# Performance work log

Measured on AMD Instinct MI355X. Metric: run time of the kernel, lower is better.

The kernel has to match this reference:

```python
import jax, jax.numpy as jnp
import numpy as np

T, B, UNITS, ACTIONS = 128, 16, 128, 6
NORM_SCALE = float(np.sqrt(UNITS))  # norm_scale = sqrt(urnn_units)


def _conv(x, w, b, stride):
    y = jax.lax.conv_general_dilated(x, w, (stride, stride), 'VALID',
                                     dimension_numbers=('NCHW', 'OIHW', 'NCHW'))
    return jax.nn.relu(y + b[None, :, None, None])


def setup_inputs() -> dict:
    key = jax.random.key(0)
    ks = jax.random.split(key, 16)
    rn = lambda k, s, sc=0.05: jax.random.normal(k, s, jnp.float32) * sc
    return {
        'x': jax.random.uniform(ks[0], (T * B, 84, 84, 3), jnp.float32, 0.0, 255.0),
        'done': (jax.random.uniform(ks[1], (T * B,)) < 0.1).astype(jnp.float32),
        'urnn_state_real': jnp.ones((B, UNITS), jnp.float32),
        'urnn_state_imag': jnp.zeros((B, UNITS), jnp.float32),
        'conv1_w': rn(ks[2], (32, 3, 8, 8)), 'conv1_b': jnp.zeros((32,), jnp.float32),
        'conv2_w': rn(ks[3], (64, 32, 4, 4)), 'conv2_b': jnp.zeros((64,), jnp.float32),
        'conv3_w': rn(ks[4], (64, 64, 3, 3)), 'conv3_b': jnp.zeros((64,), jnp.float32),
        'fc_w': rn(ks[5], (3136, 512)), 'fc_b': jnp.zeros((512,), jnp.float32),
        'win_r': rn(ks[6], (512, UNITS)), 'win_i': rn(ks[7], (512, UNITS)),
        'wrec_r': rn(ks[8], (UNITS, UNITS)), 'wrec_i': rn(ks[9], (UNITS, UNITS)),
        'actor_w': rn(ks[10], (2 * UNITS, ACTIONS), 0.01), 'actor_b': jnp.zeros((ACTIONS,), jnp.float32),
        'critic_w': rn(ks[11], (2 * UNITS, 1)), 'critic_b': jnp.zeros((1,), jnp.float32),
    }


def reference(x, done, urnn_state_real, urnn_state_imag,
              conv1_w, conv1_b, conv2_w, conv2_b, conv3_w, conv3_b,
              fc_w, fc_b, win_r, win_i, wrec_r, wrec_i,
              actor_w, actor_b, critic_w, critic_b):
    # CNN backbone (Nature-DQN) on NHWC frames scaled to [0,1]
    h = jnp.transpose(x, (0, 3, 1, 2)) / 255.0
    h = _conv(h, conv1_w, conv1_b, 4)      # [N,32,20,20]
    h = _conv(h, conv2_w, conv2_b, 2)      # [N,64,9,9]
    h = _conv(h, conv3_w, conv3_b, 1)      # [N,64,7,7]
    h = h.reshape(h.shape[0], -1)          # [N,3136]
    h = jax.nn.relu(h @ fc_w + fc_b)       # [N,512]

    h = h.reshape(T, B, -1)
    d = done.reshape(T, B)
    win = win_r + 1j * win_i               # [512,U] complex input projection
    wrec = wrec_r + 1j * wrec_i            # [U,U] complex recurrent matrix
    init = jnp.ones((B, UNITS), jnp.complex64)  # initial_hidden, ||.|| = sqrt(U)
    state0 = (urnn_state_real + 1j * urnn_state_imag).astype(jnp.complex64)

    def step(state, hd):
        ht, dt = hd
        reset = (1.0 - dt)[:, None]
        st = reset * state + (1.0 - reset) * init   # reset-mask blending
        pre = st @ wrec + ht.astype(jnp.complex64) @ win
        norm = jnp.sqrt(jnp.sum(pre.real ** 2 + pre.imag ** 2, axis=-1, keepdims=True))
        new = pre * (NORM_SCALE / norm).astype(jnp.complex64)  # renorm to sqrt(U)
        return new, new

    _, hs = jax.lax.scan(step, state0, (h, d))      # hs: [T,B,U] complex
    hs = hs.reshape(T * B, UNITS)
    hreal = jnp.concatenate([hs.real, hs.imag], axis=-1)  # [T*B, 2U]
    logits = hreal @ actor_w + actor_b
    value = hreal @ critic_w + critic_b
    return jnp.concatenate([logits, value], axis=-1)  # [T*B, ACTIONS+1]
```

## Files before the change

kernel.cpp:

```cpp
#include <hip/hip_runtime.h>
#include <hip/hip_bf16.h>

#define N_FRAMES 2048
#define T_STEPS  128
#define BATCH    16
#define UNITS    128
#define NORM_SCALE 11.313708498984760390f

typedef short bf16x8 __attribute__((ext_vector_type(8)));
typedef float f32x4 __attribute__((ext_vector_type(4)));

static __device__ inline unsigned short f2bf(float f) {
    __hip_bfloat16 h = __float2bfloat16(f);
    return __builtin_bit_cast(unsigned short, h);
}

static const size_t OFF_W1P   = 0;
static const size_t OFF_W2P   = 6144;
static const size_t OFF_W3P   = 38912;
static const size_t OFF_FCWP  = 75776;
static const size_t OFF_WSC   = 894976;
static const size_t OFF_HSR   = 1681408;
static const size_t OFF_PROJR = 2205696;
static const size_t OFF_H     = 2729984;
static const size_t OFF_Y2    = 3778560;
static const size_t OFF_Y1    = 14395392;
static const size_t OFF_Y3    = OFF_Y1;

__global__ void permute_w1mf(const float* __restrict__ w, unsigned short* __restrict__ o) {
    int i = blockIdx.x * 256 + threadIdx.x;
    if (i >= 8192) return;
    int j = i & 7; int lane = (i >> 3) & 63; int nt = (i >> 9) & 1; int ky = i >> 10;
    int t = (lane >> 4) * 8 + j;
    int oc = nt * 16 + (lane & 15);
    float v = 0.f;
    if (t < 24) {
        int kx = t / 3, ic = t % 3;
        v = w[((oc * 3 + ic) * 8 + ky) * 8 + kx] * (1.0f / 255.0f);
    }
    o[i] = f2bf(v);
}
__global__ void permute_w2mf(const float* __restrict__ w, unsigned short* __restrict__ o) {
    int i = blockIdx.x * 256 + threadIdx.x;
    if (i >= 32768) return;
    int j = i & 7; int lane = (i >> 3) & 63; int nt = (i >> 9) & 3; int kk = i >> 11;
    int ic = (lane >> 4) * 8 + j;
    int oc = nt * 16 + (lane & 15);
    int ky = kk >> 2, kx = kk & 3;
    o[i] = f2bf(w[((oc * 32 + ic) * 4 + ky) * 4 + kx]);
}
__global__ void permute_w3mf(const float* __restrict__ w, unsigned short* __restrict__ o) {
    int i = blockIdx.x * 256 + threadIdx.x;
    if (i >= 36864) return;
    int j = i & 7; int lane = (i >> 3) & 63; int nt = (i >> 9) & 3; int c = (i >> 11) & 1; int kk = i >> 12;
    int ic = c * 32 + (lane >> 4) * 8 + j;
    int oc = nt * 16 + (lane & 15);
    int ky = kk / 3, kx = kk % 3;
    o[i] = f2bf(w[((oc * 64 + ic) * 3 + ky) * 3 + kx]);
}
__global__ void permute_fcwmf(const float* __restrict__ w, unsigned short* __restrict__ o) {
    int i = blockIdx.x * 256 + threadIdx.x;
    if (i >= 1638400) return;
    int jj = i & 7; int lane = (i >> 3) & 63; int ntg = (i >> 9) & 31; int kk = i >> 14;
    int k = kk * 32 + (lane >> 4) * 8 + jj;
    int n = ntg * 16 + (lane & 15);
    float v = 0.f;
    if (k < 3136) {
        int p = k >> 6, c = k & 63;
        v = w[(size_t)(c * 49 + p) * 512 + n];
    }
    o[i] = f2bf(v);
}
__global__ void permute_wscan(const float* __restrict__ wr, const float* __restrict__ wi,
                              unsigned short* __restrict__ o) {
    int i = blockIdx.x * 256 + threadIdx.x;
    if (i >= 32768) return;
    int j = i & 7; int lane = (i >> 3) & 63; int ks = (i >> 9) & 3; int nt = (i >> 11) & 7;
    int comp = i >> 14;
    int k = ks * 32 + (lane >> 4) * 8 + j;
    int n = nt * 16 + (lane & 15);
    const float* src = comp ? wi : wr;
    o[i] = f2bf(src[k * 128 + n]);
}

__global__ __launch_bounds__(256) void conv1_kernel(const float* __restrict__ x,
                                                    const unsigned short* __restrict__ wmf,
                                                    const float* __restrict__ b,
                                                    unsigned short* __restrict__ y) {
    __shared__ unsigned short xs[11096];
    int tid = threadIdx.x;
    int blk = blockIdx.x;
    int n = blk >> 1, hb = blk & 1;

    const float4* xb4 = reinterpret_cast<const float4*>(x + (size_t)n * 21168 + hb * 40 * 252);
#pragma unroll
    for (int it = 0; it < 11; ++it) {
        int i = it * 256 + tid;
        if (i < 2772) {
            float4 v = xb4[i];
            ushort4 h;
            h.x = f2bf(v.x); h.y = f2bf(v.y); h.z = f2bf(v.z); h.w = f2bf(v.w);
            *reinterpret_cast<ushort4*>(&xs[i * 4]) = h;
        }
    }
    if (tid < 8) xs[11088 + tid] = 0;
    __syncthreads();

    int lane = tid & 63;
    int wv = tid >> 6;
    int row = lane & 15;
    int seg = lane >> 4;
    const uint4* wm = reinterpret_cast<const uint4*>(wmf);
    float b0 = b[row];
    float b1 = b[16 + row];
    int pbase = n * 400 + hb * 200;

    for (int tile = wv; tile < 13; tile += 4) {
        int p = tile * 16 + row; if (p > 199) p = 199;
        int eb = (p / 20) * 1008 + (p % 20) * 12 + seg * 8;
        f32x4 acc0 = {0.f, 0.f, 0.f, 0.f};
        f32x4 acc1 = {0.f, 0.f, 0.f, 0.f};
#pragma unroll
        for (int ky = 0; ky < 8; ++ky) {
            int ea = eb + ky * 252;
            ushort4 lo = *reinterpret_cast<const ushort4*>(&xs[ea]);
            ushort4 hi = *reinterpret_cast<const ushort4*>(&xs[ea + 4]);
            bf16x8 a = {(short)lo.x, (short)lo.y, (short)lo.z, (short)lo.w,
                        (short)hi.x, (short)hi.y, (short)hi.z, (short)hi.w};
            bf16x8 w0 = __builtin_bit_cast(bf16x8, wm[(ky * 2 + 0) * 64 + lane]);
            bf16x8 w1 = __builtin_bit_cast(bf16x8, wm[(ky * 2 + 1) * 64 + lane]);
            acc0 = __builtin_amdgcn_mfma_f32_16x16x32_bf16(a, w0, acc0, 0, 0, 0);
            acc1 = __builtin_amdgcn_mfma_f32_16x16x32_bf16(a, w1, acc1, 0, 0, 0);
        }
#pragma unroll
        for (int r = 0; r < 4; ++r) {
            int pl = tile * 16 + seg * 4 + r;
            if (pl < 200) {
                unsigned short* yp = y + ((size_t)(pbase + pl)) * 32 + row;
                yp[0]  = f2bf(fmaxf(acc0[r] + b0, 0.f));
                yp[16] = f2bf(fmaxf(acc1[r] + b1, 0.f));
            }
        }
    }
}

__global__ __launch_bounds__(256) void conv2_kernel(const unsigned short* __restrict__ y1b,
                                                    const unsigned short* __restrict__ wt,
                                                    const float* __restrict__ b,
                                                    unsigned short* __restrict__ y2) {
    __shared__ unsigned short xs[2 * 12800];
    int tid = threadIdx.x;
    int n0 = blockIdx.x * 2;
    const uint4* xg = reinterpret_cast<const uint4*>(y1b + (size_t)n0 * 12800);
    uint4* xs4 = reinterpret_cast<uint4*>(xs);
#pragma unroll
    for (int q = 0; q < 13; ++q) {
        int i = q * 256 + tid;
        if (i < 3200) {
            uint4 v = xg[i];
            int swz = (i & ~3) | ((i & 3) ^ ((i >> 3) & 3));
            xs4[swz] = v;
        }
    }
    __syncthreads();

    int lane = tid & 63;
    int wv = tid >> 6;
    int img = wv >> 1;
    int tbase = (wv & 1) * 3;
    int row = lane & 15, seg = lane >> 4;
    int imgb = img * 1600;

    int ibase[3];
#pragma unroll
    for (int t = 0; t < 3; ++t) {
        int p = (tbase + t) * 16 + row; if (p > 80) p = 80;
        ibase[t] = (p / 9) * 40 + (p % 9) * 2;
    }
    const uint4* B4 = reinterpret_cast<const uint4*>(wt);
    f32x4 acc[3][4];
#pragma unroll
    for (int t = 0; t < 3; ++t)
#pragma unroll
        for (int nt = 0; nt < 4; ++nt) acc[t][nt] = (f32x4){0.f, 0.f, 0.f, 0.f};

#pragma unroll 1
    for (int kk = 0; kk < 16; ++kk) {
        int ky = kk >> 2, kx = kk & 3;
        int koff = ky * 20 + kx;
        bf16x8 bb[4];
#pragma unroll
        for (int nt = 0; nt < 4; ++nt)
            bb[nt] = __builtin_bit_cast(bf16x8, B4[(kk * 4 + nt) * 64 + lane]);
        bf16x8 a[3];
#pragma unroll
        for (int t = 0; t < 3; ++t) {
            int ipx = ibase[t] + koff;
            int a16 = imgb + ipx * 4 + (seg ^ ((ipx >> 1) & 3));
            a[t] = __builtin_bit_cast(bf16x8, *reinterpret_cast<const uint4*>(&xs[a16 * 8]));
        }
#pragma unroll
        for (int t = 0; t < 3; ++t)
#pragma unroll
            for (int nt = 0; nt < 4; ++nt)
                acc[t][nt] = __builtin_amdgcn_mfma_f32_16x16x32_bf16(a[t], bb[nt], acc[t][nt], 0, 0, 0);
    }

#pragma unroll
    for (int nt = 0; nt < 4; ++nt) {
        int c = nt * 16 + row;
        float bc = b[c];
#pragma unroll
        for (int t = 0; t < 3; ++t)
#pragma unroll
            for (int r = 0; r < 4; ++r) {
                int p = (tbase + t) * 16 + seg * 4 + r;
                if (p < 81)
                    y2[((size_t)(n0 + img) * 81 + p) * 64 + c] = f2bf(fmaxf(acc[t][nt][r] + bc, 0.f));
            }
    }
}

__global__ __launch_bounds__(256) void conv3_kernel(const unsigned short* __restrict__ y2b,
                                                    const unsigned short* __restrict__ wt,
                                                    const float* __restrict__ b,
                                                    unsigned short* __restrict__ y3) {
    __shared__ unsigned short xs[2 * 5184];
    int tid = threadIdx.x;
    int n0 = blockIdx.x * 2;
    const uint4* xg = reinterpret_cast<const uint4*>(y2b + (size_t)n0 * 5184);
    uint4* xs4 = reinterpret_cast<uint4*>(xs);
#pragma unroll
    for (int q = 0; q < 6; ++q) {
        int i = q * 256 + tid;
        if (i < 1296) {
            uint4 v = xg[i];
            int px = i >> 3, qq = i & 7;
            xs4[px * 8 + (qq ^ (px & 7))] = v;
        }
    }
    __syncthreads();

    int lane = tid & 63;
    int wv = tid >> 6;
    int img = wv >> 1;
    int tbase = (wv & 1) * 2;
    int row = lane & 15, seg = lane >> 4;

    int ibase[2];
#pragma unroll
    for (int t = 0; t < 2; ++t) {
        int p = (tbase + t) * 16 + row; if (p > 48) p = 48;
        ibase[t] = img * 81 + (p / 7) * 9 + (p % 7);
    }
    const uint4* B4 = reinterpret_cast<const uint4*>(wt);
    f32x4 acc[2][4];
#pragma unroll
    for (int t = 0; t < 2; ++t)
#pragma unroll
        for (int nt = 0; nt < 4; ++nt) acc[t][nt] = (f32x4){0.f, 0.f, 0.f, 0.f};

#pragma unroll 1
    for (int kk = 0; kk < 9; ++kk) {
        int ky = kk / 3, kx = kk % 3;
        int koff = ky * 9 + kx;
#pragma unroll
        for (int c = 0; c < 2; ++c) {
            bf16x8 bb[4];
#pragma unroll
            for (int nt = 0; nt < 4; ++nt)
                bb[nt] = __builtin_bit_cast(bf16x8, B4[((kk * 2 + c) * 4 + nt) * 64 + lane]);
            bf16x8 a[2];
#pragma unroll
            for (int t = 0; t < 2; ++t) {
                int px = ibase[t] + koff;
                int u16 = px * 8 + ((c * 4 + seg) ^ (px & 7));
                a[t] = __builtin_bit_cast(bf16x8, *reinterpret_cast<const uint4*>(&xs[u16 * 8]));
            }
#pragma unroll
            for (int t = 0; t < 2; ++t)
#pragma unroll
                for (int nt = 0; nt < 4; ++nt)
                    acc[t][nt] = __builtin_amdgcn_mfma_f32_16x16x32_bf16(a[t], bb[nt], acc[t][nt], 0, 0, 0);
        }
    }

#pragma unroll
    for (int nt = 0; nt < 4; ++nt) {
        int c = nt * 16 + row;
        float bc = b[c];
#pragma unroll
        for (int t = 0; t < 2; ++t)
#pragma unroll
            for (int r = 0; r < 4; ++r) {
                int p = (tbase + t) * 16 + seg * 4 + r;
                if (p < 49)
                    y3[(size_t)(n0 + img) * 3136 + p * 64 + c] = f2bf(fmaxf(acc[t][nt][r] + bc, 0.f));
            }
    }
}

__global__ __launch_bounds__(256) void fc_kernel(const unsigned short* __restrict__ A,
                                                 const unsigned short* __restrict__ Bt,
                                                 const float* __restrict__ bias,
                                                 float* __restrict__ C) {
    __shared__ float Cs[64][65];
    int tid = threadIdx.x;
    int lane = tid & 63;
    int wv = tid >> 6;
    int bm = blockIdx.x & 31;
    int bn = blockIdx.x >> 5;
    int row = lane & 15, seg = lane >> 4;

    const uint4* B4 = reinterpret_cast<const uint4*>(Bt);
    f32x4 acc[4][4];
#pragma unroll
    for (int mf = 0; mf < 4; ++mf)
#pragma unroll
        for (int nf = 0; nf < 4; ++nf) acc[mf][nf] = (f32x4){0.f, 0.f, 0.f, 0.f};

    const unsigned short* Abase = A + (size_t)(bm * 64 + row) * 3136 + seg * 8;

#pragma unroll 1
    for (int kk = wv; kk < 100; kk += 4) {
        bf16x8 a[4], bb[4];
#pragma unroll
        for (int mf = 0; mf < 4; ++mf)
            a[mf] = __builtin_bit_cast(bf16x8,
                *reinterpret_cast<const uint4*>(Abase + (size_t)mf * 16 * 3136 + kk * 32));
#pragma unroll
        for (int nf = 0; nf < 4; ++nf)
            bb[nf] = __builtin_bit_cast(bf16x8, B4[(kk * 32 + bn * 4 + nf) * 64 + lane]);
#pragma unroll
        for (int mf = 0; mf < 4; ++mf)
#pragma unroll
            for (int nf = 0; nf < 4; ++nf)
                acc[mf][nf] = __builtin_amdgcn_mfma_f32_16x16x32_bf16(a[mf], bb[nf], acc[mf][nf], 0, 0, 0);
    }

#pragma unroll 1
    for (int w = 0; w < 4; ++w) {
        if (wv == w) {
#pragma unroll
            for (int mf = 0; mf < 4; ++mf)
#pragma unroll
                for (int nf = 0; nf < 4; ++nf)
#pragma unroll
                    for (int r = 0; r < 4; ++r) {
                        int rr = mf * 16 + seg * 4 + r;
                        int cc = nf * 16 + row;
                        if (w == 0) Cs[rr][cc] = acc[mf][nf][r];
                        else        Cs[rr][cc] += acc[mf][nf][r];
                    }
        }
        __syncthreads();
    }

    int r = tid >> 2, cq = (tid & 3) * 16;
#pragma unroll
    for (int q = 0; q < 4; ++q) {
        int c0 = cq + q * 4;
        float4 v = *reinterpret_cast<float4*>(&Cs[r][c0]);
        float4 bv = *reinterpret_cast<const float4*>(&bias[bn * 64 + c0]);
        v.x = fmaxf(v.x + bv.x, 0.f);
        v.y = fmaxf(v.y + bv.y, 0.f);
        v.z = fmaxf(v.z + bv.z, 0.f);
        v.w = fmaxf(v.w + bv.w, 0.f);
        *reinterpret_cast<float4*>(&C[(size_t)(bm * 64 + r) * 512 + bn * 64 + c0]) = v;
    }
}

__global__ __launch_bounds__(256) void proj_kernel(const float* __restrict__ h,
                                                   const float* __restrict__ winr,
                                                   const float* __restrict__ wini,
                                                   float2* __restrict__ pj) {
    int idx = blockIdx.x * 256 + threadIdx.x;
    int u = idx & 127;
    int n0 = (idx >> 7) * 8;
    float ar[8] = {}, ai[8] = {};
    for (int k = 0; k < 512; ++k) {
        float wrv = winr[k * 128 + u], wiv = wini[k * 128 + u];
#pragma unroll
        for (int g = 0; g < 8; ++g) {
            float hv = h[(size_t)(n0 + g) * 512 + k];
            ar[g] = fmaf(hv, wrv, ar[g]);
            ai[g] = fmaf(hv, wiv, ai[g]);
        }
    }
#pragma unroll
    for (int g = 0; g < 8; ++g)
        pj[(size_t)(n0 + g) * 128 + u] = make_float2(ar[g], ai[g]);
}

__global__ __launch_bounds__(512, 2) void scan_kernel(const float* __restrict__ done,
                                                      const float* __restrict__ sr0,
                                                      const float* __restrict__ si0,
                                                      const unsigned short* __restrict__ wsc,
                                                      const float2* __restrict__ pj,
                                                      float2* __restrict__ hs) {
    __shared__ __align__(16) unsigned short stR[2048], stI[2048];
    __shared__ __align__(16) float npart[16][8];
    int tid = threadIdx.x;
    int lane = tid & 63, wv = tid >> 6;
    int row = lane & 15, seg = lane >> 4;
    int u = wv * 16 + row;

    const uint4* W4 = reinterpret_cast<const uint4*>(wsc);
    bf16x8 WR[4], WI[4];
#pragma unroll
    for (int ks = 0; ks < 4; ++ks) {
        WR[ks] = __builtin_bit_cast(bf16x8, W4[((0 * 8 + wv) * 4 + ks) * 64 + lane]);
        WI[ks] = __builtin_bit_cast(bf16x8, W4[((1 * 8 + wv) * 4 + ks) * 64 + lane]);
    }

    for (int e = tid; e < 2048; e += 512) {
        int uu = e & 127, b = e >> 7;
        float d = done[b];
        float sr = sr0[b * 128 + uu], si = si0[b * 128 + uu];
        float bsr = (1.f - d) * sr + d;
        float bsi = (1.f - d) * si;
        int sw = ((uu >> 3) ^ (b & 15));
        stR[b * 128 + sw * 8 + (uu & 7)] = f2bf(bsr);
        stI[b * 128 + sw * 8 + (uu & 7)] = f2bf(bsi);
    }
    __syncthreads();

    float2 pjc[4];
#pragma unroll
    for (int r = 0; r < 4; ++r) {
        int b = seg * 4 + r;
        pjc[r] = pj[(size_t)(0 * 16 + b) * 128 + u];
    }

    for (int t = 0; t < T_STEPS; ++t) {
        float2 pjn[4];
        float dn[4];
        int tn = (t + 1 < T_STEPS) ? t + 1 : 127;
#pragma unroll
        for (int r = 0; r < 4; ++r) {
            int b = seg * 4 + r;
            pjn[r] = pj[(size_t)(tn * 16 + b) * 128 + u];
            dn[r] = (t + 1 < T_STEPS) ? done[(t + 1) * 16 + b] : 0.f;
        }

        bf16x8 aR[4], aI[4], aIn[4];
#pragma unroll
        for (int ks = 0; ks < 4; ++ks) {
            int unit = (ks * 4 + seg) ^ row;
            aR[ks] = __builtin_bit_cast(bf16x8,
                *reinterpret_cast<const uint4*>(&stR[row * 128 + unit * 8]));
            uint4 vi = *reinterpret_cast<const uint4*>(&stI[row * 128 + unit * 8]);
            aI[ks] = __builtin_bit_cast(bf16x8, vi);
            uint4 vn = {vi.x ^ 0x80008000u, vi.y ^ 0x80008000u,
                        vi.z ^ 0x80008000u, vi.w ^ 0x80008000u};
            aIn[ks] = __builtin_bit_cast(bf16x8, vn);
        }

        f32x4 accR = {0.f, 0.f, 0.f, 0.f};
        f32x4 accI = {0.f, 0.f, 0.f, 0.f};
#pragma unroll
        for (int ks = 0; ks < 4; ++ks) {
            accR = __builtin_amdgcn_mfma_f32_16x16x32_bf16(aR[ks], WR[ks], accR, 0, 0, 0);
            accR = __builtin_amdgcn_mfma_f32_16x16x32_bf16(aIn[ks], WI[ks], accR, 0, 0, 0);
            accI = __builtin_amdgcn_mfma_f32_16x16x32_bf16(aR[ks], WI[ks], accI, 0, 0, 0);
            accI = __builtin_amdgcn_mfma_f32_16x16x32_bf16(aI[ks], WR[ks], accI, 0, 0, 0);
        }

        float prer[4], prei[4], sq[4];
#pragma unroll
        for (int r = 0; r < 4; ++r) {
            prer[r] = accR[r] + pjc[r].x;
            prei[r] = accI[r] + pjc[r].y;
            sq[r] = fmaf(prer[r], prer[r], prei[r] * prei[r]);
        }
#pragma unroll
        for (int off = 1; off <= 8; off <<= 1) {
#pragma unroll
            for (int r = 0; r < 4; ++r) sq[r] += __shfl_xor(sq[r], off);
        }
        if (row == 0) {
#pragma unroll
            for (int r = 0; r < 4; ++r) npart[seg * 4 + r][wv] = sq[r];
        }
        __syncthreads();

        float scale[4];
#pragma unroll
        for (int r = 0; r < 4; ++r) {
            const float4* np4 = reinterpret_cast<const float4*>(&npart[seg * 4 + r][0]);
            float4 n0 = np4[0], n1 = np4[1];
            float nm = ((n0.x + n0.y) + (n0.z + n0.w)) + ((n1.x + n1.y) + (n1.z + n1.w));
            scale[r] = NORM_SCALE * rsqrtf(nm);
        }
#pragma unroll
        for (int r = 0; r < 4; ++r) {
            int b = seg * 4 + r;
            float nr = prer[r] * scale[r];
            float ni = prei[r] * scale[r];
            hs[(size_t)(t * 16 + b) * 128 + u] = make_float2(nr, ni);
            float bsr = (1.f - dn[r]) * nr + dn[r];
            float bsi = (1.f - dn[r]) * ni;
            int sw = ((u >> 3) ^ (b & 15));
            stR[b * 128 + sw * 8 + (u & 7)] = f2bf(bsr);
            stI[b * 128 + sw * 8 + (u & 7)] = f2bf(bsi);
        }
        __syncthreads();
#pragma unroll
        for (int r = 0; r < 4; ++r) pjc[r] = pjn[r];
    }
}

__global__ void heads_kernel(const float2* __restrict__ hs,
                             const float* __restrict__ aw, const float* __restrict__ ab,
                             const float* __restrict__ cw, const float* __restrict__ cb,
                             float* __restrict__ out) {
    int idx = blockIdx.x * 256 + threadIdx.x;
    if (idx >= N_FRAMES * 7) return;
    int j = idx % 7;
    int n = idx / 7;
    const float2* hp = hs + (size_t)n * 128;
    float acc;
    if (j < 6) {
        acc = ab[j];
        for (int k = 0; k < 128; ++k) {
            float2 v = hp[k];
            acc = fmaf(v.x, aw[k * 6 + j], acc);
            acc = fmaf(v.y, aw[(128 + k) * 6 + j], acc);
        }
    } else {
        acc = cb[0];
        for (int k = 0; k < 128; ++k) {
            float2 v = hp[k];
            acc = fmaf(v.x, cw[k], acc);
            acc = fmaf(v.y, cw[128 + k], acc);
        }
    }
    out[idx] = acc;
}

extern "C" void kernel_launch(void* const* d_in, const int* in_sizes, int n_in,
                              void* d_out, int out_size, void* d_ws, size_t ws_size,
                              hipStream_t stream) {
    const float* x        = (const float*)d_in[0];
    const float* done     = (const float*)d_in[1];
    const float* sr0      = (const float*)d_in[2];
    const float* si0      = (const float*)d_in[3];
    const float* conv1_w  = (const float*)d_in[4];
    const float* conv1_b  = (const float*)d_in[5];
    const float* conv2_w  = (const float*)d_in[6];
    const float* conv2_b  = (const float*)d_in[7];
    const float* conv3_w  = (const float*)d_in[8];
    const float* conv3_b  = (const float*)d_in[9];
    const float* fc_w     = (const float*)d_in[10];
    const float* fc_b     = (const float*)d_in[11];
    const float* win_r    = (const float*)d_in[12];
    const float* win_i    = (const float*)d_in[13];
    const float* wrec_r   = (const float*)d_in[14];
    const float* wrec_i   = (const float*)d_in[15];
    const float* actor_w  = (const float*)d_in[16];
    const float* actor_b  = (const float*)d_in[17];
    const float* critic_w = (const float*)d_in[18];
    const float* critic_b = (const float*)d_in[19];

    float* ws = (float*)d_ws;
    unsigned short* w1mf = (unsigned short*)(ws + OFF_W1P);
    unsigned short* w2mf = (unsigned short*)(ws + OFF_W2P);
    unsigned short* w3mf = (unsigned short*)(ws + OFF_W3P);
    unsigned short* fcb = (unsigned short*)(ws + OFF_FCWP);
    unsigned short* wsc = (unsigned short*)(ws + OFF_WSC);
    float2* hs  = (float2*)(ws + OFF_HSR);
    float2* pj  = (float2*)(ws + OFF_PROJR);
    float* h    = ws + OFF_H;
    unsigned short* y2b = (unsigned short*)(ws + OFF_Y2);
    unsigned short* y1b = (unsigned short*)(ws + OFF_Y1);
    unsigned short* y3b = (unsigned short*)(ws + OFF_Y3);
    float* outp = (float*)d_out;

    hipLaunchKernelGGL(permute_w1mf, dim3(32), dim3(256), 0, stream, conv1_w, w1mf);
    hipLaunchKernelGGL(permute_w2mf, dim3(128), dim3(256), 0, stream, conv2_w, w2mf);
    hipLaunchKernelGGL(permute_w3mf, dim3(144), dim3(256), 0, stream, conv3_w, w3mf);
    hipLaunchKernelGGL(permute_fcwmf, dim3(6400), dim3(256), 0, stream, fc_w, fcb);
    hipLaunchKernelGGL(permute_wscan, dim3(128), dim3(256), 0, stream, wrec_r, wrec_i, wsc);

    hipLaunchKernelGGL(conv1_kernel, dim3(4096), dim3(256), 0, stream, x, w1mf, conv1_b, y1b);
    hipLaunchKernelGGL(conv2_kernel, dim3(1024), dim3(256), 0, stream, y1b, w2mf, conv2_b, y2b);
    hipLaunchKernelGGL(conv3_kernel, dim3(1024), dim3(256), 0, stream, y2b, w3mf, conv3_b, y3b);
    hipLaunchKernelGGL(fc_kernel, dim3(256), dim3(256), 0, stream, y3b, fcb, fc_b, h);
    hipLaunchKernelGGL(proj_kernel, dim3(128), dim3(256), 0, stream, h, win_r, win_i, pj);
    hipLaunchKernelGGL(scan_kernel, dim3(1), dim3(512), 0, stream,
                       done, sr0, si0, wsc, pj, hs);
    hipLaunchKernelGGL(heads_kernel, dim3(56), dim3(256), 0, stream,
                       hs, actor_w, actor_b, critic_w, critic_b, outp);
}
```

Measured before the change: 407.4 us.

## Halve scan block to 4 waves, each computing two 16-unit column tiles

```diff
diff --git a/kernel.cpp b/kernel.cpp
--- a/kernel.cpp
+++ b/kernel.cpp
@@ -392,55 +392,67 @@
         pj[(size_t)(n0 + g) * 128 + u] = make_float2(ar[g], ai[g]);
 }
 
-__global__ __launch_bounds__(512, 2) void scan_kernel(const float* __restrict__ done,
+__global__ __launch_bounds__(256, 1) void scan_kernel(const float* __restrict__ done,
                                                       const float* __restrict__ sr0,
                                                       const float* __restrict__ si0,
                                                       const unsigned short* __restrict__ wsc,
                                                       const float2* __restrict__ pj,
                                                       float2* __restrict__ hs) {
     __shared__ __align__(16) unsigned short stR[2048], stI[2048];
-    __shared__ __align__(16) float npart[16][8];
+    __shared__ __align__(16) float npart[16][4];
+    __shared__ float done_l[2048];
     int tid = threadIdx.x;
     int lane = tid & 63, wv = tid >> 6;
     int row = lane & 15, seg = lane >> 4;
-    int u = wv * 16 + row;
+    int u0 = wv * 32 + row;
+    int u1 = u0 + 16;
+
+    for (int e = tid; e < 2048; e += 256) done_l[e] = done[e];
 
     const uint4* W4 = reinterpret_cast<const uint4*>(wsc);
-    bf16x8 WR[4], WI[4];
+    bf16x8 WR0[4], WI0[4], WR1[4], WI1[4];
 #pragma unroll
     for (int ks = 0; ks < 4; ++ks) {
-        WR[ks] = __builtin_bit_cast(bf16x8, W4[((0 * 8 + wv) * 4 + ks) * 64 + lane]);
-        WI[ks] = __builtin_bit_cast(bf16x8, W4[((1 * 8 + wv) * 4 + ks) * 64 + lane]);
-    }
-
-    for (int e = tid; e < 2048; e += 512) {
+        WR0[ks] = __builtin_bit_cast(bf16x8, W4[((0 * 8 + 2 * wv) * 4 + ks) * 64 + lane]);
+        WR1[ks] = __builtin_bit_cast(bf16x8, W4[((0 * 8 + 2 * wv + 1) * 4 + ks) * 64 + lane]);
+        WI0[ks] = __builtin_bit_cast(bf16x8, W4[((1 * 8 + 2 * wv) * 4 + ks) * 64 + lane]);
+        WI1[ks] = __builtin_bit_cast(bf16x8, W4[((1 * 8 + 2 * wv + 1) * 4 + ks) * 64 + lane]);
+    }
+    asm volatile("" : "+v"(WR0[0]), "+v"(WR0[1]), "+v"(WR0[2]), "+v"(WR0[3]));
+    asm volatile("" : "+v"(WR1[0]), "+v"(WR1[1]), "+v"(WR1[2]), "+v"(WR1[3]));
+    asm volatile("" : "+v"(WI0[0]), "+v"(WI0[1]), "+v"(WI0[2]), "+v"(WI0[3]));
+    asm volatile("" : "+v"(WI1[0]), "+v"(WI1[1]), "+v"(WI1[2]), "+v"(WI1[3]));
+
+    for (int e = tid; e < 2048; e += 256) {
         int uu = e & 127, b = e >> 7;
         float d = done[b];
         float sr = sr0[b * 128 + uu], si = si0[b * 128 + uu];
         float bsr = (1.f - d) * sr + d;
         float bsi = (1.f - d) * si;
-        int sw = ((uu >> 3) ^ (b & 15));
+        int sw = ((uu >> 3) ^ b);
         stR[b * 128 + sw * 8 + (uu & 7)] = f2bf(bsr);
         stI[b * 128 + sw * 8 + (uu & 7)] = f2bf(bsi);
     }
     __syncthreads();
 
-    float2 pjc[4];
+    float2 pjc0[4], pjc1[4];
 #pragma unroll
     for (int r = 0; r < 4; ++r) {
         int b = seg * 4 + r;
-        pjc[r] = pj[(size_t)(0 * 16 + b) * 128 + u];
+        pjc0[r] = pj[(size_t)b * 128 + u0];
+        pjc1[r] = pj[(size_t)b * 128 + u1];
     }
 
     for (int t = 0; t < T_STEPS; ++t) {
-        float2 pjn[4];
+        float2 pjn0[4], pjn1[4];
         float dn[4];
         int tn = (t + 1 < T_STEPS) ? t + 1 : 127;
 #pragma unroll
         for (int r = 0; r < 4; ++r) {
             int b = seg * 4 + r;
-            pjn[r] = pj[(size_t)(tn * 16 + b) * 128 + u];
-            dn[r] = (t + 1 < T_STEPS) ? done[(t + 1) * 16 + b] : 0.f;
+            pjn0[r] = pj[(size_t)(tn * 16 + b) * 128 + u0];
+            pjn1[r] = pj[(size_t)(tn * 16 + b) * 128 + u1];
+            dn[r] = (t + 1 < T_STEPS) ? done_l[(t + 1) * 16 + b] : 0.f;
         }
 
         bf16x8 aR[4], aI[4], aIn[4];
@@ -456,22 +468,30 @@
             aIn[ks] = __builtin_bit_cast(bf16x8, vn);
         }
 
-        f32x4 accR = {0.f, 0.f, 0.f, 0.f};
-        f32x4 accI = {0.f, 0.f, 0.f, 0.f};
+        f32x4 accR0 = {0.f, 0.f, 0.f, 0.f}, accI0 = {0.f, 0.f, 0.f, 0.f};
+        f32x4 accR1 = {0.f, 0.f, 0.f, 0.f}, accI1 = {0.f, 0.f, 0.f, 0.f};
 #pragma unroll
         for (int ks = 0; ks < 4; ++ks) {
-            accR = __builtin_amdgcn_mfma_f32_16x16x32_bf16(aR[ks], WR[ks], accR, 0, 0, 0);
-            accR = __builtin_amdgcn_mfma_f32_16x16x32_bf16(aIn[ks], WI[ks], accR, 0, 0, 0);
-            accI = __builtin_amdgcn_mfma_f32_16x16x32_bf16(aR[ks], WI[ks], accI, 0, 0, 0);
-            accI = __builtin_amdgcn_mfma_f32_16x16x32_bf16(aI[ks], WR[ks], accI, 0, 0, 0);
-        }
-
-        float prer[4], prei[4], sq[4];
+            accR0 = __builtin_amdgcn_mfma_f32_16x16x32_bf16(aR[ks], WR0[ks], accR0, 0, 0, 0);
+            accR0 = __builtin_amdgcn_mfma_f32_16x16x32_bf16(aIn[ks], WI0[ks], accR0, 0, 0, 0);
+            accI0 = __builtin_amdgcn_mfma_f32_16x16x32_bf16(aR[ks], WI0[ks], accI0, 0, 0, 0);
+            accI0 = __builtin_amdgcn_mfma_f32_16x16x32_bf16(aI[ks], WR0[ks], accI0, 0, 0, 0);
+            accR1 = __builtin_amdgcn_mfma_f32_16x16x32_bf16(aR[ks], WR1[ks], accR1, 0, 0, 0);
+            accR1 = __builtin_amdgcn_mfma_f32_16x16x32_bf16(aIn[ks], WI1[ks], accR1, 0, 0, 0);
+            accI1 = __builtin_amdgcn_mfma_f32_16x16x32_bf16(aR[ks], WI1[ks], accI1, 0, 0, 0);
+            accI1 = __builtin_amdgcn_mfma_f32_16x16x32_bf16(aI[ks], WR1[ks], accI1, 0, 0, 0);
+        }
+
+        float prer0[4], prei0[4], prer1[4], prei1[4], sq[4];
 #pragma unroll
         for (int r = 0; r < 4; ++r) {
-            prer[r] = accR[r] + pjc[r].x;
-            prei[r] = accI[r] + pjc[r].y;
-            sq[r] = fmaf(prer[r], prer[r], prei[r] * prei[r]);
+            prer0[r] = accR0[r] + pjc0[r].x;
+            prei0[r] = accI0[r] + pjc0[r].y;
+            prer1[r] = accR1[r] + pjc1[r].x;
+            prei1[r] = accI1[r] + pjc1[r].y;
+            float s0 = fmaf(prer0[r], prer0[r], prei0[r] * prei0[r]);
+            float s1 = fmaf(prer1[r], prer1[r], prei1[r] * prei1[r]);
+            sq[r] = s0 + s1;
         }
 #pragma unroll
         for (int off = 1; off <= 8; off <<= 1) {
@@ -484,29 +504,27 @@
         }
         __syncthreads();
 
-        float scale[4];
-#pragma unroll
-        for (int r = 0; r < 4; ++r) {
-            const float4* np4 = reinterpret_cast<const float4*>(&npart[seg * 4 + r][0]);
-            float4 n0 = np4[0], n1 = np4[1];
-            float nm = ((n0.x + n0.y) + (n0.z + n0.w)) + ((n1.x + n1.y) + (n1.z + n1.w));
-            scale[r] = NORM_SCALE * rsqrtf(nm);
-        }
 #pragma unroll
         for (int r = 0; r < 4; ++r) {
             int b = seg * 4 + r;
-            float nr = prer[r] * scale[r];
-            float ni = prei[r] * scale[r];
-            hs[(size_t)(t * 16 + b) * 128 + u] = make_float2(nr, ni);
-            float bsr = (1.f - dn[r]) * nr + dn[r];
-            float bsi = (1.f - dn[r]) * ni;
-            int sw = ((u >> 3) ^ (b & 15));
-            stR[b * 128 + sw * 8 + (u & 7)] = f2bf(bsr);
-            stI[b * 128 + sw * 8 + (u & 7)] = f2bf(bsi);
+            float4 np = *reinterpret_cast<const float4*>(&npart[b][0]);
+            float nm = (np.x + np.y) + (np.z + np.w);
+            float scale = NORM_SCALE * rsqrtf(nm);
+            float nr0 = prer0[r] * scale, ni0 = prei0[r] * scale;
+            float nr1 = prer1[r] * scale, ni1 = prei1[r] * scale;
+            hs[(size_t)(t * 16 + b) * 128 + u0] = make_float2(nr0, ni0);
+            hs[(size_t)(t * 16 + b) * 128 + u1] = make_float2(nr1, ni1);
+            float rr = 1.f - dn[r];
+            int sw0 = ((u0 >> 3) ^ b);
+            int sw1 = ((u1 >> 3) ^ b);
+            stR[b * 128 + sw0 * 8 + (u0 & 7)] = f2bf(rr * nr0 + dn[r]);
+            stI[b * 128 + sw0 * 8 + (u0 & 7)] = f2bf(rr * ni0);
+            stR[b * 128 + sw1 * 8 + (u1 & 7)] = f2bf(rr * nr1 + dn[r]);
+            stI[b * 128 + sw1 * 8 + (u1 & 7)] = f2bf(rr * ni1);
         }
         __syncthreads();
 #pragma unroll
-        for (int r = 0; r < 4; ++r) pjc[r] = pjn[r];
+        for (int r = 0; r < 4; ++r) { pjc0[r] = pjn0[r]; pjc1[r] = pjn1[r]; }
     }
 }
 
@@ -587,7 +605,7 @@
     hipLaunchKernelGGL(conv3_kernel, dim3(1024), dim3(256), 0, stream, y2b, w3mf, conv3_b, y3b);
     hipLaunchKernelGGL(fc_kernel, dim3(256), dim3(256), 0, stream, y3b, fcb, fc_b, h);
     hipLaunchKernelGGL(proj_kernel, dim3(128), dim3(256), 0, stream, h, win_r, win_i, pj);
-    hipLaunchKernelGGL(scan_kernel, dim3(1), dim3(512), 0, stream,
+    hipLaunchKernelGGL(scan_kernel, dim3(1), dim3(256), 0, stream,
                        done, sr0, si0, wsc, pj, hs);
     hipLaunchKernelGGL(heads_kernel, dim3(56), dim3(256), 0, stream,
                        hs, actor_w, actor_b, critic_w, critic_b, outp);
```

After: 396.3 us. 1.03x faster.

## Run recurrent scan in a single wavefront holding all recurrent weights in registers

Applied to the files above, without the earlier changes.

```diff
diff --git a/kernel.cpp b/kernel.cpp
--- a/kernel.cpp
+++ b/kernel.cpp
@@ -13,6 +13,10 @@
 static __device__ inline unsigned short f2bf(float f) {
     __hip_bfloat16 h = __float2bfloat16(f);
     return __builtin_bit_cast(unsigned short, h);
+}
+static __device__ inline float bf2f(unsigned short u) {
+    unsigned int x = ((unsigned int)u) << 16;
+    return __builtin_bit_cast(float, x);
 }
 
 static const size_t OFF_W1P   = 0;
@@ -75,12 +79,12 @@
                               unsigned short* __restrict__ o) {
     int i = blockIdx.x * 256 + threadIdx.x;
     if (i >= 32768) return;
-    int j = i & 7; int lane = (i >> 3) & 63; int ks = (i >> 9) & 3; int nt = (i >> 11) & 7;
+    int j = i & 7; int lane = (i >> 3) & 63; int ks = (i >> 9) & 3; int mt = (i >> 11) & 7;
     int comp = i >> 14;
     int k = ks * 32 + (lane >> 4) * 8 + j;
-    int n = nt * 16 + (lane & 15);
+    int u = mt * 16 + (lane & 15);
     const float* src = comp ? wi : wr;
-    o[i] = f2bf(src[k * 128 + n]);
+    o[i] = f2bf(src[k * 128 + u]);
 }
 
 __global__ __launch_bounds__(256) void conv1_kernel(const float* __restrict__ x,
@@ -373,7 +377,7 @@
 __global__ __launch_bounds__(256) void proj_kernel(const float* __restrict__ h,
                                                    const float* __restrict__ winr,
                                                    const float* __restrict__ wini,
-                                                   float2* __restrict__ pj) {
+                                                   unsigned int* __restrict__ pj) {
     int idx = blockIdx.x * 256 + threadIdx.x;
     int u = idx & 127;
     int n0 = (idx >> 7) * 8;
@@ -389,124 +393,143 @@
     }
 #pragma unroll
     for (int g = 0; g < 8; ++g)
-        pj[(size_t)(n0 + g) * 128 + u] = make_float2(ar[g], ai[g]);
-}
-
-__global__ __launch_bounds__(512, 2) void scan_kernel(const float* __restrict__ done,
-                                                      const float* __restrict__ sr0,
-                                                      const float* __restrict__ si0,
-                                                      const unsigned short* __restrict__ wsc,
-                                                      const float2* __restrict__ pj,
-                                                      float2* __restrict__ hs) {
-    __shared__ __align__(16) unsigned short stR[2048], stI[2048];
-    __shared__ __align__(16) float npart[16][8];
-    int tid = threadIdx.x;
-    int lane = tid & 63, wv = tid >> 6;
-    int row = lane & 15, seg = lane >> 4;
-    int u = wv * 16 + row;
+        pj[(size_t)(n0 + g) * 128 + u] = (unsigned int)f2bf(ar[g]) | ((unsigned int)f2bf(ai[g]) << 16);
+}
+
+__global__ __launch_bounds__(64, 1) void scan_kernel(const float* __restrict__ done,
+                                                     const float* __restrict__ sr0,
+                                                     const float* __restrict__ si0,
+                                                     const unsigned short* __restrict__ wsc,
+                                                     const unsigned int* __restrict__ pj,
+                                                     float2* __restrict__ hs) {
+    __shared__ __align__(16) unsigned int stR[1024], stI[1024];
+    __shared__ float done_l[2048];
+    int lane = threadIdx.x;
+    int b = lane & 15, seg = lane >> 4;
+    int swz = (b & 3) << 3;
 
     const uint4* W4 = reinterpret_cast<const uint4*>(wsc);
-    bf16x8 WR[4], WI[4];
-#pragma unroll
-    for (int ks = 0; ks < 4; ++ks) {
-        WR[ks] = __builtin_bit_cast(bf16x8, W4[((0 * 8 + wv) * 4 + ks) * 64 + lane]);
-        WI[ks] = __builtin_bit_cast(bf16x8, W4[((1 * 8 + wv) * 4 + ks) * 64 + lane]);
-    }
-
-    for (int e = tid; e < 2048; e += 512) {
-        int uu = e & 127, b = e >> 7;
-        float d = done[b];
-        float sr = sr0[b * 128 + uu], si = si0[b * 128 + uu];
-        float bsr = (1.f - d) * sr + d;
-        float bsi = (1.f - d) * si;
-        int sw = ((uu >> 3) ^ (b & 15));
-        stR[b * 128 + sw * 8 + (uu & 7)] = f2bf(bsr);
-        stI[b * 128 + sw * 8 + (uu & 7)] = f2bf(bsi);
-    }
-    __syncthreads();
-
-    float2 pjc[4];
-#pragma unroll
-    for (int r = 0; r < 4; ++r) {
-        int b = seg * 4 + r;
-        pjc[r] = pj[(size_t)(0 * 16 + b) * 128 + u];
-    }
+    bf16x8 WR[8][4], WI[8][4];
+#pragma unroll
+    for (int mt = 0; mt < 8; ++mt)
+#pragma unroll
+        for (int ks = 0; ks < 4; ++ks) {
+            WR[mt][ks] = __builtin_bit_cast(bf16x8, W4[((0 * 8 + mt) * 4 + ks) * 64 + lane]);
+            WI[mt][ks] = __builtin_bit_cast(bf16x8, W4[((1 * 8 + mt) * 4 + ks) * 64 + lane]);
+        }
+#pragma unroll
+    for (int mt = 0; mt < 8; ++mt) {
+        asm volatile("" : "+v"(WR[mt][0]), "+v"(WR[mt][1]), "+v"(WR[mt][2]), "+v"(WR[mt][3]));
+        asm volatile("" : "+v"(WI[mt][0]), "+v"(WI[mt][1]), "+v"(WI[mt][2]), "+v"(WI[mt][3]));
+    }
+
+    for (int e = lane; e < 2048; e += 64) done_l[e] = done[e];
+
+    for (int p = lane; p < 1024; p += 64) {
+        int bb = p >> 6, upair = p & 63;
+        int u0 = upair * 2;
+        float d = done[bb];
+        float rr = 1.f - d;
+        float sr0v = rr * sr0[bb * 128 + u0] + d;
+        float sr1v = rr * sr0[bb * 128 + u0 + 1] + d;
+        float si0v = rr * si0[bb * 128 + u0];
+        float si1v = rr * si0[bb * 128 + u0 + 1];
+        int addr = bb * 64 + (upair ^ ((bb & 3) << 3));
+        stR[addr] = (unsigned int)f2bf(sr0v) | ((unsigned int)f2bf(sr1v) << 16);
+        stI[addr] = (unsigned int)f2bf(si0v) | ((unsigned int)f2bf(si1v) << 16);
+    }
+
+    uint4 pjc[8];
+#pragma unroll
+    for (int mt = 0; mt < 8; ++mt)
+        pjc[mt] = *reinterpret_cast<const uint4*>(&pj[(size_t)b * 128 + mt * 16 + seg * 4]);
 
     for (int t = 0; t < T_STEPS; ++t) {
-        float2 pjn[4];
-        float dn[4];
-        int tn = (t + 1 < T_STEPS) ? t + 1 : 127;
-#pragma unroll
-        for (int r = 0; r < 4; ++r) {
-            int b = seg * 4 + r;
-            pjn[r] = pj[(size_t)(tn * 16 + b) * 128 + u];
-            dn[r] = (t + 1 < T_STEPS) ? done[(t + 1) * 16 + b] : 0.f;
-        }
-
-        bf16x8 aR[4], aI[4], aIn[4];
+        asm volatile("s_waitcnt lgkmcnt(0)" ::: "memory");
+        __builtin_amdgcn_sched_barrier(0);
+
+        bf16x8 SBr[4], SBi[4], SBin[4];
 #pragma unroll
         for (int ks = 0; ks < 4; ++ks) {
-            int unit = (ks * 4 + seg) ^ row;
-            aR[ks] = __builtin_bit_cast(bf16x8,
-                *reinterpret_cast<const uint4*>(&stR[row * 128 + unit * 8]));
-            uint4 vi = *reinterpret_cast<const uint4*>(&stI[row * 128 + unit * 8]);
-            aI[ks] = __builtin_bit_cast(bf16x8, vi);
+            int addr = b * 64 + ((ks * 16 + seg * 4) ^ swz);
+            uint4 vr = *reinterpret_cast<const uint4*>(&stR[addr]);
+            uint4 vi = *reinterpret_cast<const uint4*>(&stI[addr]);
+            SBr[ks] = __builtin_bit_cast(bf16x8, vr);
+            SBi[ks] = __builtin_bit_cast(bf16x8, vi);
             uint4 vn = {vi.x ^ 0x80008000u, vi.y ^ 0x80008000u,
                         vi.z ^ 0x80008000u, vi.w ^ 0x80008000u};
-            aIn[ks] = __builtin_bit_cast(bf16x8, vn);
-        }
-
-        f32x4 accR = {0.f, 0.f, 0.f, 0.f};
-        f32x4 accI = {0.f, 0.f, 0.f, 0.f};
-#pragma unroll
-        for (int ks = 0; ks < 4; ++ks) {
-            accR = __builtin_amdgcn_mfma_f32_16x16x32_bf16(aR[ks], WR[ks], accR, 0, 0, 0);
-            accR = __builtin_amdgcn_mfma_f32_16x16x32_bf16(aIn[ks], WI[ks], accR, 0, 0, 0);
-            accI = __builtin_amdgcn_mfma_f32_16x16x32_bf16(aR[ks], WI[ks], accI, 0, 0, 0);
-            accI = __builtin_amdgcn_mfma_f32_16x16x32_bf16(aI[ks], WR[ks], accI, 0, 0, 0);
-        }
-
-        float prer[4], prei[4], sq[4];
-#pragma unroll
-        for (int r = 0; r < 4; ++r) {
-            prer[r] = accR[r] + pjc[r].x;
-            prei[r] = accI[r] + pjc[r].y;
-            sq[r] = fmaf(prer[r], prer[r], prei[r] * prei[r]);
-        }
-#pragma unroll
-        for (int off = 1; off <= 8; off <<= 1) {
-#pragma unroll
-            for (int r = 0; r < 4; ++r) sq[r] += __shfl_xor(sq[r], off);
-        }
-        if (row == 0) {
-#pragma unroll
-            for (int r = 0; r < 4; ++r) npart[seg * 4 + r][wv] = sq[r];
-        }
-        __syncthreads();
-
-        float scale[4];
-#pragma unroll
-        for (int r = 0; r < 4; ++r) {
-            const float4* np4 = reinterpret_cast<const float4*>(&npart[seg * 4 + r][0]);
-            float4 n0 = np4[0], n1 = np4[1];
-            float nm = ((n0.x + n0.y) + (n0.z + n0.w)) + ((n1.x + n1.y) + (n1.z + n1.w));
-            scale[r] = NORM_SCALE * rsqrtf(nm);
-        }
-#pragma unroll
-        for (int r = 0; r < 4; ++r) {
-            int b = seg * 4 + r;
-            float nr = prer[r] * scale[r];
-            float ni = prei[r] * scale[r];
-            hs[(size_t)(t * 16 + b) * 128 + u] = make_float2(nr, ni);
-            float bsr = (1.f - dn[r]) * nr + dn[r];
-            float bsi = (1.f - dn[r]) * ni;
-            int sw = ((u >> 3) ^ (b & 15));
-            stR[b * 128 + sw * 8 + (u & 7)] = f2bf(bsr);
-            stI[b * 128 + sw * 8 + (u & 7)] = f2bf(bsi);
-        }
-        __syncthreads();
-#pragma unroll
-        for (int r = 0; r < 4; ++r) pjc[r] = pjn[r];
+            SBin[ks] = __builtin_bit_cast(bf16x8, vn);
+        }
+
+        f32x4 accR[8], accI[8];
+#pragma unroll
+        for (int mt = 0; mt < 8; ++mt) {
+            accR[mt] = (f32x4){0.f, 0.f, 0.f, 0.f};
+            accI[mt] = (f32x4){0.f, 0.f, 0.f, 0.f};
+        }
+#pragma unroll
+        for (int ks = 0; ks < 4; ++ks)
+#pragma unroll
+            for (int mt = 0; mt < 8; ++mt) {
+                accR[mt] = __builtin_amdgcn_mfma_f32_16x16x32_bf16(WR[mt][ks], SBr[ks], accR[mt], 0, 0, 0);
+                accR[mt] = __builtin_amdgcn_mfma_f32_16x16x32_bf16(WI[mt][ks], SBin[ks], accR[mt], 0, 0, 0);
+                accI[mt] = __builtin_amdgcn_mfma_f32_16x16x32_bf16(WR[mt][ks], SBi[ks], accI[mt], 0, 0, 0);
+                accI[mt] = __builtin_amdgcn_mfma_f32_16x16x32_bf16(WI[mt][ks], SBr[ks], accI[mt], 0, 0, 0);
+            }
+
+        float prer[8][4], prei[8][4];
+        float sq = 0.f;
+#pragma unroll
+        for (int mt = 0; mt < 8; ++mt) {
+            unsigned int pw[4] = {pjc[mt].x, pjc[mt].y, pjc[mt].z, pjc[mt].w};
+#pragma unroll
+            for (int r = 0; r < 4; ++r) {
+                float pr_ = bf2f((unsigned short)(pw[r] & 0xffff));
+                float pi_ = bf2f((unsigned short)(pw[r] >> 16));
+                prer[mt][r] = accR[mt][r] + pr_;
+                prei[mt][r] = accI[mt][r] + pi_;
+                sq = fmaf(prer[mt][r], prer[mt][r], sq);
+                sq = fmaf(prei[mt][r], prei[mt][r], sq);
+            }
+        }
+        sq += __shfl_xor(sq, 16);
+        sq += __shfl_xor(sq, 32);
+        float scale = NORM_SCALE * rsqrtf(sq);
+
+        int tn = (t + 1 < T_STEPS) ? t + 1 : 127;
+        uint4 pjn[8];
+#pragma unroll
+        for (int mt = 0; mt < 8; ++mt)
+            pjn[mt] = *reinterpret_cast<const uint4*>(&pj[(size_t)(tn * 16 + b) * 128 + mt * 16 + seg * 4]);
+
+        float dn = (t + 1 < T_STEPS) ? done_l[(t + 1) * 16 + b] : 0.f;
+        float rr = 1.f - dn;
+
+#pragma unroll
+        for (int mt = 0; mt < 8; ++mt) {
+            float nr[4], ni[4];
+#pragma unroll
+            for (int r = 0; r < 4; ++r) {
+                nr[r] = prer[mt][r] * scale;
+                ni[r] = prei[mt][r] * scale;
+            }
+            float4 h0 = {nr[0], ni[0], nr[1], ni[1]};
+            float4 h1 = {nr[2], ni[2], nr[3], ni[3]};
+            float* hp = reinterpret_cast<float*>(&hs[(size_t)(t * 16 + b) * 128 + mt * 16 + seg * 4]);
+            *reinterpret_cast<float4*>(hp) = h0;
+            *reinterpret_cast<float4*>(hp + 4) = h1;
+            unsigned int p0 = (unsigned int)f2bf(fmaf(rr, nr[0], dn)) |
+                              ((unsigned int)f2bf(fmaf(rr, nr[1], dn)) << 16);
+            unsigned int p1 = (unsigned int)f2bf(fmaf(rr, nr[2], dn)) |
+                              ((unsigned int)f2bf(fmaf(rr, nr[3], dn)) << 16);
+            unsigned int q0 = (unsigned int)f2bf(rr * ni[0]) | ((unsigned int)f2bf(rr * ni[1]) << 16);
+            unsigned int q1 = (unsigned int)f2bf(rr * ni[2]) | ((unsigned int)f2bf(rr * ni[3]) << 16);
+            int addr = b * 64 + ((mt * 8 + seg * 2) ^ swz);
+            *reinterpret_cast<uint2*>(&stR[addr]) = make_uint2(p0, p1);
+            *reinterpret_cast<uint2*>(&stI[addr]) = make_uint2(q0, q1);
+        }
+#pragma unroll
+        for (int mt = 0; mt < 8; ++mt) pjc[mt] = pjn[mt];
     }
 }
 
@@ -569,7 +592,7 @@
     unsigned short* fcb = (unsigned short*)(ws + OFF_FCWP);
     unsigned short* wsc = (unsigned short*)(ws + OFF_WSC);
     float2* hs  = (float2*)(ws + OFF_HSR);
-    float2* pj  = (float2*)(ws + OFF_PROJR);
+    unsigned int* pj = (unsigned int*)(ws + OFF_PROJR);
     float* h    = ws + OFF_H;
     unsigned short* y2b = (unsigned short*)(ws + OFF_Y2);
     unsigned short* y1b = (unsigned short*)(ws + OFF_Y1);
@@ -587,7 +610,7 @@
     hipLaunchKernelGGL(conv3_kernel, dim3(1024), dim3(256), 0, stream, y2b, w3mf, conv3_b, y3b);
     hipLaunchKernelGGL(fc_kernel, dim3(256), dim3(256), 0, stream, y3b, fcb, fc_b, h);
     hipLaunchKernelGGL(proj_kernel, dim3(128), dim3(256), 0, stream, h, win_r, win_i, pj);
-    hipLaunchKernelGGL(scan_kernel, dim3(1), dim3(512), 0, stream,
+    hipLaunchKernelGGL(scan_kernel, dim3(1), dim3(64), 0, stream,
                        done, sr0, si0, wsc, pj, hs);
     hipLaunchKernelGGL(heads_kernel, dim3(56), dim3(256), 0, stream,
                        hs, actor_w, actor_b, critic_w, critic_b, outp);
```

Result: slower. 498.7 us (+22.4%).
